# Kernel optimization log

Hardware: AMD Instinct MI355X
Metric: run time of the kernel (lower is better)

Reference implementation:

```python
import jax, jax.numpy as jnp
import numpy as np

T, D, F, E, K = 8192, 1024, 4096, 8, 2


def setup_inputs() -> dict:
    key = jax.random.key(0)
    ks = jax.random.split(key, 8)
    s = 0.02
    return {
        "gate_inputs": jax.random.normal(ks[0], (T, D), jnp.float32),
        "inputs": jax.random.normal(ks[1], (T, D), jnp.float32),
        "Wg": jax.random.normal(ks[2], (D, E), jnp.float32) * s,
        "bg": jnp.zeros((E,), jnp.float32),
        "w1": jax.random.normal(ks[3], (E, D, F), jnp.float32) * s,
        "b1": jnp.zeros((E, F), jnp.float32),
        "w2": jax.random.normal(ks[4], (E, F, D), jnp.float32) * s,
        "b2": jnp.zeros((E, D), jnp.float32),
    }


def reference(gate_inputs, inputs, Wg, bg, w1, b1, w2, b2):
    # gate + top-k routing (torch.topk returns sorted descending, as lax.top_k)
    logits = gate_inputs @ Wg + bg                      # [T, E]
    weights, selected = jax.lax.top_k(logits, K)        # [T, K]
    weights = jax.nn.softmax(weights.astype(jnp.float32), axis=1).astype(inputs.dtype)
    # scatter top-k weights into dense combine matrix [T, E]
    t_idx = jnp.arange(inputs.shape[0])[:, None]
    combine = jnp.zeros(logits.shape, inputs.dtype).at[t_idx, selected].add(weights)

    # loop over experts via scan (E is a small structural dim), accumulate weighted outputs
    def body(acc, params):
        W1, B1, W2, B2, ce = params                     # ce: [T] combine weight for this expert
        h = jax.nn.gelu(inputs @ W1 + B1)               # [T, F]
        y = h @ W2 + B2                                 # [T, D]
        return acc + ce[:, None] * y, None

    out, _ = jax.lax.scan(body, jnp.zeros_like(inputs), (w1, b1, w2, b2, combine.T))
    return out
```

## Files before the change

### kernel.cpp

```cpp
#include <hip/hip_runtime.h>
#include <stdint.h>

#define T_TOK 8192
#define DMODEL 1024
#define FDIM 4096
#define NEXP 8
#define NROWS 16384
#define MAXT 80

#define GATE_BLKS 2048
#define CVT_BLKS  4096
#define TRP_BLKS  2048
#define PREP_BLKS (GATE_BLKS + CVT_BLKS + TRP_BLKS)

typedef __bf16 bf16x8 __attribute__((ext_vector_type(8)));
typedef float f32x4 __attribute__((ext_vector_type(4)));
#define AS1 __attribute__((address_space(1)))
#define AS3 __attribute__((address_space(3)))

__device__ __forceinline__ unsigned short f2bf(float f) {
  union { float f; unsigned u; } v; v.f = f;
  unsigned r = v.u + 0x7fffu + ((v.u >> 16) & 1u);
  return (unsigned short)(r >> 16);
}
__device__ __forceinline__ float bflo(unsigned u) {
  union { unsigned u; float f; } v; v.u = u << 16; return v.f;
}
__device__ __forceinline__ float bfhi(unsigned u) {
  union { unsigned u; float f; } v; v.u = u & 0xffff0000u; return v.f;
}

__device__ __forceinline__ void tile_tr_pipe(
    const float* __restrict__ in, unsigned short* __restrict__ out,
    int Kdim, int Ndim, int e, int kt, int ng0, float* lds)
{
  size_t ebase = (size_t)e * Kdim * Ndim;
  const int tid = threadIdx.x, lane = tid & 63, wave = tid >> 6;
  const int lr = lane >> 4, lc = (lane & 15) * 4;
  auto stage = [&](int i, int b) {
    const int n0 = (ng0 + i) * 64;
#pragma unroll
    for (int it = 0; it < 4; ++it) {
      int c = wave * 4 + it;
      const float* src = in + ebase + (size_t)(kt * 64 + c * 4 + lr) * Ndim + n0 + lc;
      __builtin_amdgcn_global_load_lds(
          (const AS1 void*)src,
          (AS3 void*)((char*)lds + b * 16384 + c * 1024), 16, 0, 0);
    }
  };
  stage(0, 0);
  for (int i = 0; i < 8; ++i) {
    const int b = i & 1;
    if (i + 1 < 8) {
      stage(i + 1, b ^ 1);
      asm volatile("s_waitcnt vmcnt(4)" ::: "memory");
    } else {
      asm volatile("s_waitcnt vmcnt(0)" ::: "memory");
    }
    __syncthreads();
    const float* L = lds + b * 4096;
    int n = tid >> 2, k16 = (tid & 3) * 16;
    union { unsigned short h[16]; uint4 q[2]; } pk;
#pragma unroll
    for (int j = 0; j < 16; ++j)
      pk.h[j] = f2bf(L[(k16 + j) * 64 + n]);
    unsigned short* dst = out + ebase + ((size_t)kt * Ndim + (ng0 + i) * 64 + n) * 64 + k16;
    *(uint4*)dst = pk.q[0];
    *(uint4*)(dst + 8) = pk.q[1];
    __syncthreads();
  }
}

__global__ __launch_bounds__(256) void prep_kernel(
    const float* __restrict__ gx, const float* __restrict__ Wg,
    const float* __restrict__ bg, int* __restrict__ sel,
    float* __restrict__ wts,
    const float* __restrict__ inputs, unsigned short* __restrict__ Xb,
    const float* __restrict__ w1, unsigned short* __restrict__ W1T,
    const float* __restrict__ w2, unsigned short* __restrict__ W2T)
{
  __shared__ __align__(16) float tr_lds[2 * 64 * 64];
  int b = blockIdx.x;
  if (b < GATE_BLKS) {
    int t = b * 4 + (threadIdx.x >> 6);
    int lane = threadIdx.x & 63;
    const float* row = gx + (size_t)t * DMODEL;
    float acc[NEXP];
#pragma unroll
    for (int e = 0; e < NEXP; ++e) acc[e] = 0.f;
    for (int d = lane; d < DMODEL; d += 64) {
      float x = row[d];
      const float* wgr = Wg + (size_t)d * NEXP;
#pragma unroll
      for (int e = 0; e < NEXP; ++e) acc[e] += x * wgr[e];
    }
#pragma unroll
    for (int off = 32; off > 0; off >>= 1) {
#pragma unroll
      for (int e = 0; e < NEXP; ++e) acc[e] += __shfl_down(acc[e], off);
    }
    if (lane == 0) {
      float lg[NEXP];
#pragma unroll
      for (int e = 0; e < NEXP; ++e) lg[e] = acc[e] + bg[e];
      int i1 = 0; float v1 = lg[0];
#pragma unroll
      for (int e = 1; e < NEXP; ++e) if (lg[e] > v1) { v1 = lg[e]; i1 = e; }
      int i2 = -1; float v2 = -3.4e38f;
#pragma unroll
      for (int e = 0; e < NEXP; ++e) if (e != i1 && lg[e] > v2) { v2 = lg[e]; i2 = e; }
      float ez = __expf(v2 - v1);
      float s = 1.f / (1.f + ez);
      sel[t*2] = i1; sel[t*2+1] = i2;
      wts[t*2] = s;  wts[t*2+1] = ez * s;
    }
  } else if (b < GATE_BLKS + CVT_BLKS) {
    int i = (b - GATE_BLKS) * 256 + threadIdx.x;
    const float4* in4 = (const float4*)inputs;
    float4 v0 = in4[(size_t)i*2], v1 = in4[(size_t)i*2 + 1];
    union { unsigned short u[8]; uint4 q; } r;
    r.u[0]=f2bf(v0.x); r.u[1]=f2bf(v0.y); r.u[2]=f2bf(v0.z); r.u[3]=f2bf(v0.w);
    r.u[4]=f2bf(v1.x); r.u[5]=f2bf(v1.y); r.u[6]=f2bf(v1.z); r.u[7]=f2bf(v1.w);
    ((uint4*)Xb)[i] = r.q;
  } else {
    int bp = b - (GATE_BLKS + CVT_BLKS);
    if (bp < 1024) {
      int e = bp >> 7, rem = bp & 127;
      tile_tr_pipe(w1, W1T, DMODEL, FDIM, e, rem >> 3, (rem & 7) * 8, tr_lds);
    } else {
      bp -= 1024;
      int e = bp >> 7, rem = bp & 127;
      tile_tr_pipe(w2, W2T, FDIM, DMODEL, e, rem >> 1, (rem & 1) * 8, tr_lds);
    }
  }
}

__global__ __launch_bounds__(256) void scan_build_kernel(
    const int* __restrict__ sel, int* __restrict__ offsets,
    int* __restrict__ ntiles, int* __restrict__ t_e, int* __restrict__ t_r,
    int* __restrict__ t_rend)
{
  __shared__ int sc[8], soff[9], stile[9];
  int tid = threadIdx.x;
  if (tid < 8) sc[tid] = 0;
  __syncthreads();
  int cnt[NEXP];
#pragma unroll
  for (int e = 0; e < NEXP; ++e) cnt[e] = 0;
  for (int i = tid; i < NROWS; i += 256) {
    int v = sel[i];
#pragma unroll
    for (int e = 0; e < NEXP; ++e) cnt[e] += (v == e) ? 1 : 0;
  }
#pragma unroll
  for (int e = 0; e < NEXP; ++e) if (cnt[e]) atomicAdd(&sc[e], cnt[e]);
  __syncthreads();
  if (tid == 0) {
    int off = 0, tl = 0;
#pragma unroll
    for (int e = 0; e < NEXP; ++e) {
      soff[e] = off; stile[e] = tl;
      off += sc[e];
      tl += (sc[e] + 255) >> 8;
    }
    soff[8] = off; stile[8] = tl;
  }
  __syncthreads();
  int ntot = stile[8];
  for (int idx = tid; idx < ntot; idx += 256) {
    int e = 0;
#pragma unroll
    for (int q = 0; q < NEXP; ++q) if (idx >= stile[q + 1]) e = q + 1;
    int r = (idx - stile[e]) * 256;
    t_e[idx] = e; t_r[idx] = soff[e] + r; t_rend[idx] = soff[e] + sc[e];
  }
  if (tid < 9) offsets[tid] = soff[tid];
  if (tid == 0) *ntiles = ntot;
}

__global__ __launch_bounds__(256) void scatter_kernel(
    const int* __restrict__ sel, int* __restrict__ cursors,
    const int* __restrict__ offsets, int* __restrict__ token_list,
    int* __restrict__ slot_list)
{
  int t = blockIdx.x * 256 + threadIdx.x;
  int lane = threadIdx.x & 63;
  unsigned long long ltmask = (lane == 63) ? 0x7fffffffffffffffull
                                           : ((1ull << lane) - 1ull);
#pragma unroll
  for (int k = 0; k < 2; ++k) {
    int e = sel[t*2 + k];
#pragma unroll
    for (int ex = 0; ex < NEXP; ++ex) {
      unsigned long long m = __ballot(e == ex);
      if (m == 0ull) continue;
      if (e == ex) {
        int leader = __ffsll((unsigned long long)m) - 1;
        int cnt = __popcll(m);
        int base = 0;
        if (lane == leader) base = atomicAdd(&cursors[ex], cnt);
        base = __shfl(base, leader);
        int r = offsets[ex] + base + __popcll(m & ltmask);
        token_list[r] = t;
        slot_list[r] = t*2 + k;
      }
    }
  }
}

template<bool G1>
__global__ __launch_bounds__(512, 2) void gemm256_kernel(
    const unsigned short* __restrict__ A, const unsigned short* __restrict__ B,
    const float* __restrict__ b1, const int* __restrict__ token_list,
    const int* __restrict__ slot_list,
    const int* __restrict__ tile_e, const int* __restrict__ tile_r,
    const int* __restrict__ tile_rend, const int* __restrict__ ntiles,
    unsigned short* __restrict__ outp)
{
  constexpr int KDIM = G1 ? DMODEL : FDIM;
  constexpr int NKT  = KDIM / 64;
  constexpr int NOUT = G1 ? FDIM : DMODEL;
  constexpr int KTB  = NOUT * 64;

  int bid = blockIdx.x;
  int nb, bt;
  if constexpr (G1) {
    int xcd = bid & 7, idx = bid >> 3;
    nb = xcd * 2 + (idx & 1);
    bt = idx >> 1;
  } else {
    nb = bid & 3;
    bt = bid >> 2;
  }
  if (bt >= *ntiles) return;
  const int e = tile_e[bt], row0 = tile_r[bt], rend = tile_rend[bt];
  const int n0 = nb * 256;

  const int tid = threadIdx.x, lane = tid & 63, wave = tid >> 6;
  extern __shared__ __align__(16) char smem[];

  const int lr8 = lane >> 3, g8 = lane & 7, ch = g8 ^ lr8;

  int mA[2], mB[2];
#pragma unroll
  for (int p = 0; p < 2; ++p)
    mA[p] = (wave < 4) ? (p*64 + wave*16) : (128 + p*64 + (wave-4)*16);
#pragma unroll
  for (int nh = 0; nh < 2; ++nh)
    mB[nh] = (wave >> 1)*64 + nh*32 + (wave & 1)*16;

  const unsigned short* eB = B + (size_t)e * KDIM * NOUT;
  unsigned aoffs[2][2], boffs[2][2];
#pragma unroll
  for (int p = 0; p < 2; ++p)
#pragma unroll
    for (int l = 0; l < 2; ++l) {
      int m = mA[p] + l*8 + lr8;
      int row = row0 + m; if (row > NROWS - 1) row = NROWS - 1;
      int arow = G1 ? token_list[row] : row;
      aoffs[p][l] = (unsigned)arow * KDIM + ch*8;
      int mb = mB[p] + l*8 + lr8;
      boffs[p][l] = (unsigned)((n0 + mb) * 64 + ch*8);
    }

  auto stage_half = [&](int p, int ktn, int bsel) {
    char* base = smem + bsel * 65536;
    if (p < 2) {
      const int kb = ktn * 64;
#pragma unroll
      for (int l = 0; l < 2; ++l)
        __builtin_amdgcn_global_load_lds(
            (const AS1 void*)(A + aoffs[p][l] + kb),
            (AS3 void*)(base + ((mA[p] + l*8) << 7)), 16, 0, 0);
    } else {
      const int nh = p - 2;
      const unsigned short* bk = eB + (size_t)ktn * KTB;
#pragma unroll
      for (int l = 0; l < 2; ++l)
        __builtin_amdgcn_global_load_lds(
            (const AS1 void*)(bk + boffs[nh][l]),
            (AS3 void*)(base + 32768 + ((mB[nh] + l*8) << 7)), 16, 0, 0);
    }
  };

  f32x4 acc[8][4] = {};
  bf16x8 aR[4][2];
  bf16x8 bR[2][2][2];
  const int wr = wave >> 2, wc = wave & 3;
  const int lm = lane & 15, lk = lane >> 4, l7 = lane & 7;
  const unsigned abase = (unsigned)(wr*128 + lm) * 128;
  const unsigned bbase = 32768u + (unsigned)(wc*64 + lm) * 128;
  const unsigned kx0 = (unsigned)((lk ^ l7) << 4);
  const unsigned kx1 = (unsigned)(((4 + lk) ^ l7) << 4);

  auto rdA = [&](const char* base, int mh) {
#pragma unroll
    for (int i = 0; i < 4; ++i) {
      const char* pA = base + abase + mh*8192 + i*2048;
      aR[i][0] = *(const bf16x8*)(pA + kx0);
      aR[i][1] = *(const bf16x8*)(pA + kx1);
    }
  };
  auto rdB = [&](const char* base, int nh) {
#pragma unroll
    for (int jj = 0; jj < 2; ++jj) {
      const char* pB = base + bbase + nh*4096 + jj*2048;
      bR[nh][jj][0] = *(const bf16x8*)(pB + kx0);
      bR[nh][jj][1] = *(const bf16x8*)(pB + kx1);
    }
  };
  auto mm = [&](int mh, int nh) {
    __builtin_amdgcn_s_setprio(1);
#pragma unroll
    for (int i = 0; i < 4; ++i)
#pragma unroll
      for (int jj = 0; jj < 2; ++jj) {
        acc[mh*4+i][nh*2+jj] = __builtin_amdgcn_mfma_f32_16x16x32_bf16(
            aR[i][0], bR[nh][jj][0], acc[mh*4+i][nh*2+jj], 0, 0, 0);
        acc[mh*4+i][nh*2+jj] = __builtin_amdgcn_mfma_f32_16x16x32_bf16(
            aR[i][1], bR[nh][jj][1], acc[mh*4+i][nh*2+jj], 0, 0, 0);
      }
    __builtin_amdgcn_s_setprio(0);
  };

  stage_half(0, 0, 0);
  stage_half(2, 0, 0);
  stage_half(3, 0, 0);
  stage_half(1, 0, 0);
  asm volatile("s_waitcnt vmcnt(2)" ::: "memory");
  __builtin_amdgcn_s_barrier();
  __builtin_amdgcn_sched_barrier(0);
  rdA((const char*)smem, 0); rdB((const char*)smem, 0);
  __builtin_amdgcn_sched_barrier(0);

  for (int kt = 0; kt < NKT; ++kt) {
    const int b = kt & 1, nxt = b ^ 1;
    const char* base = smem + b * 65536;
    const char* nbase = smem + nxt * 65536;
    const bool pre = (kt + 1 < NKT);
    __builtin_amdgcn_s_barrier();
    asm volatile("s_waitcnt lgkmcnt(0)" ::: "memory");
    __builtin_amdgcn_sched_barrier(0);
    mm(0, 0);
    if (pre) {
      stage_half(0, kt + 1, nxt);
      stage_half(2, kt + 1, nxt);
      asm volatile("s_waitcnt vmcnt(4)" ::: "memory");
    } else {
      asm volatile("s_waitcnt vmcnt(0)" ::: "memory");
    }
    rdB(base, 1);
    __builtin_amdgcn_sched_barrier(0);
    __builtin_amdgcn_s_barrier();
    asm volatile("s_waitcnt lgkmcnt(0)" ::: "memory");
    __builtin_amdgcn_sched_barrier(0);
    mm(0, 1);
    if (pre) stage_half(3, kt + 1, nxt);
    rdA(base, 1);
    __builtin_amdgcn_sched_barrier(0);
    __builtin_amdgcn_s_barrier();
    asm volatile("s_waitcnt lgkmcnt(0)" ::: "memory");
    __builtin_amdgcn_sched_barrier(0);
    mm(1, 1);
    if (pre) {
      stage_half(1, kt + 1, nxt);
      asm volatile("s_waitcnt vmcnt(4)" ::: "memory");
    }
    __builtin_amdgcn_sched_barrier(0);
    __builtin_amdgcn_s_barrier();
    __builtin_amdgcn_sched_barrier(0);
    mm(1, 0);
    if (pre) {
      asm volatile("s_waitcnt vmcnt(2)" ::: "memory");
      rdA(nbase, 0); rdB(nbase, 0);
    }
    __builtin_amdgcn_sched_barrier(0);
  }

  asm volatile("" ::: "memory");
  float bias[4] = {};
  if constexpr (G1) {
#pragma unroll
    for (int j = 0; j < 4; ++j) bias[j] = b1[(size_t)e * FDIM + n0 + wc*64 + j*16 + lm];
  }

  float* eps = (float*)smem;
#pragma unroll
  for (int c = 0; c < 8; ++c) {
    __syncthreads();
    if (wr == (c >> 2)) {
#pragma unroll
      for (int ii = 0; ii < 2; ++ii) {
        const int mi = (c & 3) * 2 + ii;
#pragma unroll
        for (int j = 0; j < 4; ++j) {
#pragma unroll
          for (int r = 0; r < 4; ++r) {
            float v = acc[mi][j][r];
            if constexpr (G1) {
              v += bias[j];
              float z2 = 1.5957691216f * (v + 0.044715f * v * v * v);
              v = v / (1.f + __expf(-z2));
            }
            eps[(ii*16 + lk*4 + r) * 260 + wc*64 + j*16 + lm] = v;
          }
        }
      }
    }
    __syncthreads();
#pragma unroll
    for (int u = 0; u < 2; ++u) {
      int item = u * 512 + tid;
      int lrow = item >> 5, c8 = (item & 31) * 8;
      int gr = row0 + c * 32 + lrow;
      if (gr < rend) {
        float4 v0 = *(const float4*)&eps[lrow * 260 + c8];
        float4 v1 = *(const float4*)&eps[lrow * 260 + c8 + 4];
        union { unsigned short u[8]; uint4 q; } pk;
        pk.u[0]=f2bf(v0.x); pk.u[1]=f2bf(v0.y); pk.u[2]=f2bf(v0.z); pk.u[3]=f2bf(v0.w);
        pk.u[4]=f2bf(v1.x); pk.u[5]=f2bf(v1.y); pk.u[6]=f2bf(v1.z); pk.u[7]=f2bf(v1.w);
        size_t orow;
        if constexpr (G1) orow = (size_t)gr * FDIM;
        else              orow = (size_t)slot_list[gr] * DMODEL;
        *(uint4*)(outp + orow + n0 + c8) = pk.q;
      }
    }
  }
}

__global__ __launch_bounds__(256) void combine_kernel(
    const unsigned short* __restrict__ ys, const float* __restrict__ wts,
    const int* __restrict__ sel, const float* __restrict__ b2,
    float* __restrict__ out)
{
  int i = blockIdx.x * 256 + threadIdx.x;
  int t = i >> 7, d8 = i & 127;
  float w0 = wts[t*2], w1 = wts[t*2 + 1];
  int e0 = sel[t*2], e1 = sel[t*2 + 1];
  const uint4* ys4 = (const uint4*)ys;
  uint4 ya = ys4[(size_t)(t*2) * 128 + d8];
  uint4 yb = ys4[(size_t)(t*2 + 1) * 128 + d8];
  const float4* b24 = (const float4*)b2;
  float4 c0a = b24[e0*256 + d8*2], c0b = b24[e0*256 + d8*2 + 1];
  float4 c1a = b24[e1*256 + d8*2], c1b = b24[e1*256 + d8*2 + 1];
  float4 o0, o1;
  o0.x = w0*(bflo(ya.x)+c0a.x) + w1*(bflo(yb.x)+c1a.x);
  o0.y = w0*(bfhi(ya.x)+c0a.y) + w1*(bfhi(yb.x)+c1a.y);
  o0.z = w0*(bflo(ya.y)+c0a.z) + w1*(bflo(yb.y)+c1a.z);
  o0.w = w0*(bfhi(ya.y)+c0a.w) + w1*(bfhi(yb.y)+c1a.w);
  o1.x = w0*(bflo(ya.z)+c0b.x) + w1*(bflo(yb.z)+c1b.x);
  o1.y = w0*(bfhi(ya.z)+c0b.y) + w1*(bfhi(yb.z)+c1b.y);
  o1.z = w0*(bflo(ya.w)+c0b.z) + w1*(bflo(yb.w)+c1b.z);
  o1.w = w0*(bfhi(ya.w)+c0b.w) + w1*(bfhi(yb.w)+c1b.w);
  float4* out4 = (float4*)out;
  out4[(size_t)t * 256 + d8*2]     = o0;
  out4[(size_t)t * 256 + d8*2 + 1] = o1;
}

extern "C" void kernel_launch(void* const* d_in, const int* in_sizes, int n_in,
                              void* d_out, int out_size, void* d_ws, size_t ws_size,
                              hipStream_t stream)
{
  const float* gate_inputs = (const float*)d_in[0];
  const float* inputs      = (const float*)d_in[1];
  const float* Wg          = (const float*)d_in[2];
  const float* bg          = (const float*)d_in[3];
  const float* w1          = (const float*)d_in[4];
  const float* b1          = (const float*)d_in[5];
  const float* w2          = (const float*)d_in[6];
  const float* b2          = (const float*)d_in[7];
  float* out = (float*)d_out;

  char* ws = (char*)d_ws;
  size_t o = 0;
  auto carve = [&](size_t bytes) { void* p = ws + o; o += (bytes + 255) & ~(size_t)255; return p; };
  unsigned short* Xb  = (unsigned short*)carve((size_t)T_TOK * DMODEL * 2);
  unsigned short* W1T = (unsigned short*)carve((size_t)NEXP * FDIM * DMODEL * 2);
  unsigned short* W2T = (unsigned short*)carve((size_t)NEXP * DMODEL * FDIM * 2);
  unsigned short* H   = (unsigned short*)carve((size_t)NROWS * FDIM * 2);
  unsigned short* ys  = (unsigned short*)carve((size_t)NROWS * DMODEL * 2);
  int*   sel          = (int*)carve((size_t)NROWS * 4);
  float* wts          = (float*)carve((size_t)NROWS * 4);
  int*   token_list   = (int*)carve((size_t)(NROWS + 256) * 4);
  int*   slot_list    = (int*)carve((size_t)(NROWS + 256) * 4);
  int*   ctrl         = (int*)carve(4096);
  int* cursors = ctrl + 8;
  int* offsets = ctrl + 16;
  int* ntiles  = ctrl + 28;
  int* t_e     = ctrl + 32;
  int* t_r     = ctrl + 32 + MAXT;
  int* t_rend  = ctrl + 32 + 2 * MAXT;

  hipMemsetAsync(ctrl, 0, 64, stream);

  prep_kernel<<<PREP_BLKS, 256, 0, stream>>>(
      gate_inputs, Wg, bg, sel, wts,
      inputs, Xb, w1, W1T, w2, W2T);
  scan_build_kernel<<<1, 256, 0, stream>>>(sel, offsets, ntiles, t_e, t_r, t_rend);
  scatter_kernel<<<T_TOK / 256, 256, 0, stream>>>(sel, cursors, offsets, token_list, slot_list);

  hipFuncSetAttribute((const void*)gemm256_kernel<true>,
                      hipFuncAttributeMaxDynamicSharedMemorySize, 131072);
  hipFuncSetAttribute((const void*)gemm256_kernel<false>,
                      hipFuncAttributeMaxDynamicSharedMemorySize, 131072);
  gemm256_kernel<true><<<8 * 2 * MAXT, 512, 131072, stream>>>(
      Xb, W1T, b1, token_list, nullptr, t_e, t_r, t_rend, ntiles, H);
  gemm256_kernel<false><<<4 * MAXT, 512, 131072, stream>>>(
      H, W2T, nullptr, nullptr, slot_list, t_e, t_r, t_rend, ntiles, ys);
  combine_kernel<<<(T_TOK * DMODEL / 8) / 256, 256, 0, stream>>>(ys, wts, sel, b2, out);
}
```

Measured before the change: 586.5 us.

## Load B operand directly from global into registers, halving LDS staging

The grouped MoE GEMM no longer stages the weight (B) tile through LDS. Each wave now reads its B fragments straight from global memory into registers, prefetching the next k-step during the MFMA phases. Only the A tile is double-buffered in LDS, so dynamic shared memory drops from 128KB to 64KB and the pipeline needs fewer barriers. The trade-off is that B is no longer shared across waves through LDS, so global or L2 traffic for the weights rises, and global-load latency now sits directly in the register path, which could stall the MFMAs.

```diff
diff --git a/kernel.cpp b/kernel.cpp
--- a/kernel.cpp
+++ b/kernel.cpp
@@ -241,16 +241,12 @@
 
   const int lr8 = lane >> 3, g8 = lane & 7, ch = g8 ^ lr8;
 
-  int mA[2], mB[2];
+  int mA[2];
 #pragma unroll
   for (int p = 0; p < 2; ++p)
     mA[p] = (wave < 4) ? (p*64 + wave*16) : (128 + p*64 + (wave-4)*16);
-#pragma unroll
-  for (int nh = 0; nh < 2; ++nh)
-    mB[nh] = (wave >> 1)*64 + nh*32 + (wave & 1)*16;
-
-  const unsigned short* eB = B + (size_t)e * KDIM * NOUT;
-  unsigned aoffs[2][2], boffs[2][2];
+
+  unsigned aoffs[2][2];
 #pragma unroll
   for (int p = 0; p < 2; ++p)
 #pragma unroll
@@ -259,28 +255,18 @@
       int row = row0 + m; if (row > NROWS - 1) row = NROWS - 1;
       int arow = G1 ? token_list[row] : row;
       aoffs[p][l] = (unsigned)arow * KDIM + ch*8;
-      int mb = mB[p] + l*8 + lr8;
-      boffs[p][l] = (unsigned)((n0 + mb) * 64 + ch*8);
-    }
-
-  auto stage_half = [&](int p, int ktn, int bsel) {
-    char* base = smem + bsel * 65536;
-    if (p < 2) {
-      const int kb = ktn * 64;
+    }
+
+  auto stageA = [&](int ktn, int bsel) {
+    char* base = smem + bsel * 32768;
+    const int kb = ktn * 64;
+#pragma unroll
+    for (int p = 0; p < 2; ++p)
 #pragma unroll
       for (int l = 0; l < 2; ++l)
         __builtin_amdgcn_global_load_lds(
             (const AS1 void*)(A + aoffs[p][l] + kb),
             (AS3 void*)(base + ((mA[p] + l*8) << 7)), 16, 0, 0);
-    } else {
-      const int nh = p - 2;
-      const unsigned short* bk = eB + (size_t)ktn * KTB;
-#pragma unroll
-      for (int l = 0; l < 2; ++l)
-        __builtin_amdgcn_global_load_lds(
-            (const AS1 void*)(bk + boffs[nh][l]),
-            (AS3 void*)(base + 32768 + ((mB[nh] + l*8) << 7)), 16, 0, 0);
-    }
   };
 
   f32x4 acc[8][4] = {};
@@ -289,9 +275,19 @@
   const int wr = wave >> 2, wc = wave & 3;
   const int lm = lane & 15, lk = lane >> 4, l7 = lane & 7;
   const unsigned abase = (unsigned)(wr*128 + lm) * 128;
-  const unsigned bbase = 32768u + (unsigned)(wc*64 + lm) * 128;
   const unsigned kx0 = (unsigned)((lk ^ l7) << 4);
   const unsigned kx1 = (unsigned)(((4 + lk) ^ l7) << 4);
+
+  const unsigned short* eB = B + (size_t)e * KDIM * NOUT;
+  unsigned boffR[2][2][2];
+#pragma unroll
+  for (int nh = 0; nh < 2; ++nh)
+#pragma unroll
+    for (int jj = 0; jj < 2; ++jj)
+#pragma unroll
+      for (int ks = 0; ks < 2; ++ks)
+        boffR[nh][jj][ks] =
+            (unsigned)((n0 + wc*64 + nh*32 + jj*16 + lm) * 64 + (ks*4 + lk) * 8);
 
   auto rdA = [&](const char* base, int mh) {
 #pragma unroll
@@ -299,14 +295,6 @@
       const char* pA = base + abase + mh*8192 + i*2048;
       aR[i][0] = *(const bf16x8*)(pA + kx0);
       aR[i][1] = *(const bf16x8*)(pA + kx1);
-    }
-  };
-  auto rdB = [&](const char* base, int nh) {
-#pragma unroll
-    for (int jj = 0; jj < 2; ++jj) {
-      const char* pB = base + bbase + nh*4096 + jj*2048;
-      bR[nh][jj][0] = *(const bf16x8*)(pB + kx0);
-      bR[nh][jj][1] = *(const bf16x8*)(pB + kx1);
     }
   };
   auto mm = [&](int mh, int nh) {
@@ -323,57 +311,55 @@
     __builtin_amdgcn_s_setprio(0);
   };
 
-  stage_half(0, 0, 0);
-  stage_half(2, 0, 0);
-  stage_half(3, 0, 0);
-  stage_half(1, 0, 0);
-  asm volatile("s_waitcnt vmcnt(2)" ::: "memory");
-  __builtin_amdgcn_s_barrier();
-  __builtin_amdgcn_sched_barrier(0);
-  rdA((const char*)smem, 0); rdB((const char*)smem, 0);
-  __builtin_amdgcn_sched_barrier(0);
+  stageA(0, 0);
+  {
+    const unsigned short* bk = eB;
+#pragma unroll
+    for (int jj = 0; jj < 2; ++jj)
+#pragma unroll
+      for (int ks = 0; ks < 2; ++ks) {
+        bR[1][jj][ks] = *(const bf16x8*)(bk + boffR[1][jj][ks]);
+        bR[0][jj][ks] = *(const bf16x8*)(bk + boffR[0][jj][ks]);
+      }
+  }
 
   for (int kt = 0; kt < NKT; ++kt) {
-    const int b = kt & 1, nxt = b ^ 1;
-    const char* base = smem + b * 65536;
-    const char* nbase = smem + nxt * 65536;
     const bool pre = (kt + 1 < NKT);
+    const char* base = smem + (kt & 1) * 32768;
+    const unsigned short* bkn = eB + (size_t)(kt + 1) * KTB;
+    if (pre) {
+      stageA(kt + 1, (kt + 1) & 1);
+      asm volatile("s_waitcnt vmcnt(4)" ::: "memory");
+    } else {
+      asm volatile("s_waitcnt vmcnt(0)" ::: "memory");
+    }
     __builtin_amdgcn_s_barrier();
+    __builtin_amdgcn_sched_barrier(0);
+    rdA(base, 0);
     asm volatile("s_waitcnt lgkmcnt(0)" ::: "memory");
     __builtin_amdgcn_sched_barrier(0);
     mm(0, 0);
-    if (pre) {
-      stage_half(0, kt + 1, nxt);
-      stage_half(2, kt + 1, nxt);
-      asm volatile("s_waitcnt vmcnt(4)" ::: "memory");
-    } else {
-      asm volatile("s_waitcnt vmcnt(0)" ::: "memory");
-    }
-    rdB(base, 1);
-    __builtin_amdgcn_sched_barrier(0);
-    __builtin_amdgcn_s_barrier();
-    asm volatile("s_waitcnt lgkmcnt(0)" ::: "memory");
-    __builtin_amdgcn_sched_barrier(0);
     mm(0, 1);
-    if (pre) stage_half(3, kt + 1, nxt);
     rdA(base, 1);
-    __builtin_amdgcn_sched_barrier(0);
-    __builtin_amdgcn_s_barrier();
     asm volatile("s_waitcnt lgkmcnt(0)" ::: "memory");
     __builtin_amdgcn_sched_barrier(0);
     mm(1, 1);
     if (pre) {
-      stage_half(1, kt + 1, nxt);
-      asm volatile("s_waitcnt vmcnt(4)" ::: "memory");
-    }
-    __builtin_amdgcn_sched_barrier(0);
-    __builtin_amdgcn_s_barrier();
-    __builtin_amdgcn_sched_barrier(0);
+#pragma unroll
+      for (int jj = 0; jj < 2; ++jj)
+#pragma unroll
+        for (int ks = 0; ks < 2; ++ks)
+          bR[1][jj][ks] = *(const bf16x8*)(bkn + boffR[1][jj][ks]);
+    }
     mm(1, 0);
     if (pre) {
-      asm volatile("s_waitcnt vmcnt(2)" ::: "memory");
-      rdA(nbase, 0); rdB(nbase, 0);
-    }
+#pragma unroll
+      for (int jj = 0; jj < 2; ++jj)
+#pragma unroll
+        for (int ks = 0; ks < 2; ++ks)
+          bR[0][jj][ks] = *(const bf16x8*)(bkn + boffR[0][jj][ks]);
+    }
+    __builtin_amdgcn_s_barrier();
     __builtin_amdgcn_sched_barrier(0);
   }
 
@@ -500,12 +486,12 @@
   scatter_kernel<<<T_TOK / 256, 256, 0, stream>>>(sel, cursors, offsets, token_list, slot_list);
 
   hipFuncSetAttribute((const void*)gemm256_kernel<true>,
-                      hipFuncAttributeMaxDynamicSharedMemorySize, 131072);
+                      hipFuncAttributeMaxDynamicSharedMemorySize, 65536);
   hipFuncSetAttribute((const void*)gemm256_kernel<false>,
-                      hipFuncAttributeMaxDynamicSharedMemorySize, 131072);
-  gemm256_kernel<true><<<8 * 2 * MAXT, 512, 131072, stream>>>(
+                      hipFuncAttributeMaxDynamicSharedMemorySize, 65536);
+  gemm256_kernel<true><<<8 * 2 * MAXT, 512, 65536, stream>>>(
       Xb, W1T, b1, token_list, nullptr, t_e, t_r, t_rend, ntiles, H);
-  gemm256_kernel<false><<<4 * MAXT, 512, 131072, stream>>>(
+  gemm256_kernel<false><<<4 * MAXT, 512, 65536, stream>>>(
       H, W2T, nullptr, nullptr, slot_list, t_e, t_r, t_rend, ntiles, ys);
   combine_kernel<<<(T_TOK * DMODEL / 8) / 256, 256, 0, stream>>>(ys, wts, sel, b2, out);
 }
```

New measurement: 820.3 us. 1.4x slower.
